# Kernel optimization log

Measured on AMD Instinct MI355X. Metric: run time of the kernel, lower is better.

## Reference

```python
import jax, jax.numpy as jnp
import numpy as np

N_FEATURES = 128
N_QUBITS = 10
Q_DEPTH = 4
N_OUTPUTS = 1
BATCH = 32768


def _apply_1q(psi, U, w, n):
    """Apply a single-qubit gate on wire w. psi: [B, 2^n]; U: [2,2] or [B,2,2]."""
    B = psi.shape[0]
    left, right = 2 ** w, 2 ** (n - 1 - w)
    psi = psi.reshape(B, left, 2, right)
    if U.ndim == 2:
        psi = jnp.einsum('ij,bljr->blir', U, psi)
    else:
        psi = jnp.einsum('bij,bljr->blir', U, psi)
    return psi.reshape(B, -1)


def _apply_cnot(psi, c, t, n):
    """CNOT(control=c, target=t) on psi [B, 2^n] (wire 0 = most significant bit)."""
    B = psi.shape[0]
    psi = psi.reshape((B,) + (2,) * n)
    ax_c, ax_t = c + 1, t + 1
    psi0 = jnp.take(psi, 0, axis=ax_c)
    psi1 = jnp.take(psi, 1, axis=ax_c)
    ax_t2 = ax_t - 1 if ax_t > ax_c else ax_t  # target axis shifts after removing control axis
    psi1 = jnp.flip(psi1, axis=ax_t2)          # flip target bit where control == 1
    psi = jnp.stack([psi0, psi1], axis=ax_c)
    return psi.reshape(B, -1)


def _rx_batched(theta):
    """RX(theta) per sample. theta: [B] -> U: [B,2,2] complex64."""
    c = jnp.cos(0.5 * theta).astype(jnp.complex64)
    s = jnp.sin(0.5 * theta).astype(jnp.complex64)
    row0 = jnp.stack([c, -1j * s], axis=-1)
    row1 = jnp.stack([-1j * s, c], axis=-1)
    return jnp.stack([row0, row1], axis=-2)


def _rot(phi, theta, omega):
    """Pennylane Rot = RZ(omega) @ RY(theta) @ RZ(phi), scalar angles -> [2,2] complex64."""
    c = jnp.cos(0.5 * theta)
    s = jnp.sin(0.5 * theta)
    u00 = jnp.exp(-0.5j * (phi + omega)) * c
    u01 = -jnp.exp(0.5j * (phi - omega)) * s
    u10 = jnp.exp(-0.5j * (phi - omega)) * s
    u11 = jnp.exp(0.5j * (phi + omega)) * c
    return jnp.stack([jnp.stack([u00, u01]), jnp.stack([u10, u11])]).astype(jnp.complex64)


def _quantum_forward(angles, q_weights):
    """Batched statevector sim: AngleEmbedding(RX) + StronglyEntanglingLayers, PauliZ expvals."""
    B, n = angles.shape
    depth = q_weights.shape[0]
    D = 2 ** n
    psi = jnp.zeros((B, D), jnp.complex64).at[:, 0].set(1.0)
    # AngleEmbedding: RX(angles[:, w]) on each wire (per-sample angles)
    for w in range(n):
        psi = _apply_1q(psi, _rx_batched(angles[:, w]), w, n)
    # StronglyEntanglingLayers: Rot on each wire, then CNOT ring with range r
    for l in range(depth):
        for w in range(n):
            U = _rot(q_weights[l, w, 0], q_weights[l, w, 1], q_weights[l, w, 2])
            psi = _apply_1q(psi, U, w, n)
        r = (l % (n - 1)) + 1
        for w in range(n):
            psi = _apply_cnot(psi, w, (w + r) % n, n)
    probs = psi.real ** 2 + psi.imag ** 2  # [B, D]
    # <Z_i> = sum_k probs[:,k] * (+1 if bit_i(k)==0 else -1); wire 0 = MSB
    bits = (jnp.arange(D)[None, :] >> (n - 1 - jnp.arange(n))[:, None]) & 1  # [n, D]
    signs = (1.0 - 2.0 * bits).astype(jnp.float32)
    return probs @ signs.T  # [B, n]


def setup_inputs() -> dict:
    key = jax.random.key(0)
    ks = jax.random.split(key, 5)
    x = jax.random.normal(ks[0], (BATCH, N_FEATURES), jnp.float32)
    W_pre = jax.random.normal(ks[1], (N_QUBITS, N_FEATURES), jnp.float32) / np.sqrt(N_FEATURES).astype(np.float32)
    b_pre = jnp.zeros((N_QUBITS,), jnp.float32)
    q_weights = 0.01 * jax.random.normal(ks[2], (Q_DEPTH, N_QUBITS, 3), jnp.float32)
    W_post = jax.random.normal(ks[3], (N_OUTPUTS, N_QUBITS), jnp.float32) / np.sqrt(N_QUBITS).astype(np.float32)
    b_post = jnp.zeros((N_OUTPUTS,), jnp.float32)
    return {"x": x, "W_pre": W_pre, "b_pre": b_pre, "q_weights": q_weights, "W_post": W_post, "b_post": b_post}


def reference(x, W_pre, b_pre, q_weights, W_post, b_post):
    angles = jnp.tanh(x @ W_pre.T + b_pre)        # pre_net + tanh -> [B, n_qubits]
    q_out = _quantum_forward(angles, q_weights)   # PauliZ expectations [B, n_qubits]
    return jax.nn.sigmoid(q_out @ W_post.T + b_post)
```

## Files before the change

kernel.cpp:

```cpp
#include <hip/hip_runtime.h>
#include <math.h>

#define BATCH 32768

typedef unsigned int u32;

#if defined(__has_builtin)
#if __has_builtin(__builtin_amdgcn_permlane32_swap) && __has_builtin(__builtin_amdgcn_permlane16_swap)
#define USE_PERMLANE 1
#else
#define USE_PERMLANE 0
#endif
#if __has_builtin(__builtin_amdgcn_fdot2)
#define HAS_FDOT2 1
#else
#define HAS_FDOT2 0
#endif
#else
#define USE_PERMLANE 0
#define HAS_FDOT2 0
#endif

struct GateC { unsigned prt, sel; };
struct CircuitT { GateC g[4][10]; unsigned srow[10]; };

constexpr CircuitT make_circuit() {
  CircuitT C{};
  unsigned row[10], col[10];
  for (int b = 0; b < 10; ++b) { row[b] = 1u << b; col[b] = 1u << b; }
  for (int l = 0; l < 4; ++l) {
    for (int w = 0; w < 10; ++w) {
      C.g[l][w].prt = col[9 - w];
      C.g[l][w].sel = row[9 - w];
    }
    const int r = (l % 9) + 1;
    for (int w = 0; w < 10; ++w) {
      const int c = w, t = (w + r) % 10;
      const int bc = 9 - c, bt = 9 - t;
      row[bt] ^= row[bc];
      col[bc] ^= col[bt];
    }
  }
  for (int i = 0; i < 10; ++i) C.srow[i] = row[9 - i];
  return C;
}
constexpr CircuitT CIRC = make_circuit();

constexpr int ORD[4][10] = {
  {0,1,2,3,4,5,6,7,8,9},
  {0,6,1,7,2,8,3,4,9,5},
  {0,2,1,3,7,4,8,5,9,6},
  {0,3,1,2,4,5,6,7,8,9},
};

template<int M>
__device__ __forceinline__ u32 lshuf(u32 v, int lane, int bpa) {
  static_assert(M != 0, "mask must be nonzero");
  if constexpr ((M & 32) != 0) {
    return (u32)__builtin_amdgcn_ds_bpermute(bpa, (int)v);
  } else {
    return (u32)__builtin_amdgcn_ds_swizzle((int)v, 0x1F | (M << 10));
  }
}

template<int CTRL>
__device__ __forceinline__ float dppf(float v) {
  const int i = __float_as_int(v);
  return __int_as_float(__builtin_amdgcn_update_dpp(i, i, CTRL, 0xF, 0xF, false));
}
__device__ __forceinline__ float shflx(float v, int m) { return __shfl_xor(v, m, 64); }

__device__ __forceinline__ float wave_sum(float v, int lane) {
  v += dppf<0xB1>(v);
  v += dppf<0x4E>(v);
  v += dppf<0x141>(v);
  v += dppf<0x140>(v);
#if USE_PERMLANE
  { auto r = __builtin_amdgcn_permlane16_swap(__float_as_uint(v), __float_as_uint(v), false, false);
    v = __uint_as_float(r[0]) + __uint_as_float(r[1]); }
  { auto r = __builtin_amdgcn_permlane32_swap(__float_as_uint(v), __float_as_uint(v), false, false);
    v = __uint_as_float(r[0]) + __uint_as_float(r[1]); }
#else
  v += shflx(v, 16);
  v += shflx(v, 32);
#endif
  return v;
}

__device__ __forceinline__ float half_sum(float v) {
  v += dppf<0xB1>(v);
  v += dppf<0x4E>(v);
  v += dppf<0x141>(v);
  v += dppf<0x140>(v);
#if USE_PERMLANE
  { auto r = __builtin_amdgcn_permlane16_swap(__float_as_uint(v), __float_as_uint(v), false, false);
    v = __uint_as_float(r[0]) + __uint_as_float(r[1]); }
#else
  v += shflx(v, 16);
#endif
  return v;
}

__device__ __forceinline__ float xswapf(float v, int lane) {
#if USE_PERMLANE
  auto r = __builtin_amdgcn_permlane32_swap(__float_as_uint(v), __float_as_uint(v), false, false);
  return (lane & 32) ? __uint_as_float(r[0]) : __uint_as_float(r[1]);
#else
  return shflx(v, 32);
#endif
}

__device__ __forceinline__ u32 pk_mul_h(u32 a, u32 b) {
  u32 d; asm("v_pk_mul_f16 %0, %1, %2" : "=v"(d) : "v"(a), "v"(b)); return d;
}
__device__ __forceinline__ u32 pk_fma_h(u32 a, u32 b, u32 c) {
  u32 d; asm("v_pk_fma_f16 %0, %1, %2, %3" : "=v"(d) : "v"(a), "v"(b), "v"(c)); return d;
}
__device__ __forceinline__ u32 pk_fma_hsw(u32 a, u32 b, u32 c) {
  u32 d;
  asm("v_pk_fma_f16 %0, %1, %2, %3 op_sel:[1,0,0] op_sel_hi:[0,1,1]"
      : "=v"(d) : "v"(a), "v"(b), "v"(c));
  return d;
}
__device__ __forceinline__ u32 pk2(float lo, float hi) {
  auto h = __builtin_amdgcn_cvt_pkrtz(lo, hi);
  return __builtin_bit_cast(u32, h);
}
__device__ __forceinline__ u32 updh(u32 a, u32 q, const uint4 s) {
  u32 t = pk_mul_h(a, s.x);
  t = pk_fma_hsw(a, s.y, t);
  t = pk_fma_h(q, s.z, t);
  t = pk_fma_hsw(q, s.w, t);
  return t;
}

template<int L, int W>
__device__ __forceinline__ void gate2(u32 a0[16], u32 a1[16],
                                      const u32* __restrict__ Ush, int lane) {
  constexpr unsigned PRT = CIRC.g[L][W].prt;
  constexpr unsigned SEL = CIRC.g[L][W].sel;
  constexpr int PLm = (int)(PRT >> 4), PRm = (int)(PRT & 15u);
  constexpr int SLm = (int)(SEL >> 4), SRm = (int)(SEL & 15u);

  int hl = 0;
  if constexpr (SLm != 0) hl = __popc(lane & SLm) & 1;

  const u32* gb = Ush + (L * 10 + W - 10) * 8;
  const uint4 cA = *(const uint4*)(gb + (hl << 2));
  uint4 cB;
  if constexpr (SRm != 0) cB = *(const uint4*)(gb + ((hl ^ 1) << 2));
  else                    cB = cA;

  int bpa = 0;
  if constexpr ((PLm & 32) != 0) bpa = (lane ^ PLm) << 2;

  if constexpr (PLm == 0) {
    constexpr int LB = PRm & (-PRm);
#pragma unroll
    for (int t0 = 0; t0 < 16; ++t0) {
      if (t0 & LB) continue;
      const int t1 = t0 ^ PRm;
      const uint4 s0 = (__builtin_popcount((unsigned)(t0 & SRm)) & 1) ? cB : cA;
      const uint4 s1 = (__builtin_popcount((unsigned)(t1 & SRm)) & 1) ? cB : cA;
      const u32 x0 = a0[t0], x1 = a0[t1];
      a0[t0] = updh(x0, x1, s0);
      a0[t1] = updh(x1, x0, s1);
      const u32 y0 = a1[t0], y1 = a1[t1];
      a1[t0] = updh(y0, y1, s0);
      a1[t1] = updh(y1, y0, s1);
    }
  } else {
#pragma unroll
    for (int t = 0; t < 16; ++t) {
      const uint4 s = (__builtin_popcount((unsigned)(t & SRm)) & 1) ? cB : cA;
      const u32 q0 = lshuf<PLm>(a0[t ^ PRm], lane, bpa);
      const u32 q1 = lshuf<PLm>(a1[t ^ PRm], lane, bpa);
      a0[t] = updh(a0[t], q0, s);
      a1[t] = updh(a1[t], q1, s);
    }
  }
}

template<int L, int K>
__device__ __forceinline__ void layer2_from(u32 a0[16], u32 a1[16],
                                            const u32* __restrict__ Ush, int lane) {
  if constexpr (K < 10) {
    gate2<L, ORD[L][K]>(a0, a1, Ush, lane);
    layer2_from<L, K + 1>(a0, a1, Ush, lane);
  }
}

__device__ __forceinline__ void build_state(u32 a[16], const float cw[10], const float sw[10],
                                            const u32* __restrict__ Ush, int lane) {
  float u0r[10], u0i[10], u1r[10], u1i[10];
#pragma unroll
  for (int w = 0; w < 10; ++w) {
    const u32* q = &Ush[240 + w * 8];
    const float A = __uint_as_float(q[0]), Br = __uint_as_float(q[1]);
    const float Bi = __uint_as_float(q[2]), Cr = __uint_as_float(q[3]);
    const float Ci = __uint_as_float(q[4]), Dr = __uint_as_float(q[5]);
    const float Di = __uint_as_float(q[6]);
    const float ch = cw[w], sh = sw[w];
    u0r[w] = fmaf(A, ch, Bi * sh);
    u0i[w] = -Br * sh;
    u1r[w] = fmaf(Cr, ch, Di * sh);
    u1i[w] = fmaf(Ci, ch, -Dr * sh);
  }

  float Lr, Li;
  {
    const int b0 = (lane >> 5) & 1;
    Lr = b0 ? u1r[0] : u0r[0];
    Li = b0 ? u1i[0] : u0i[0];
  }
#pragma unroll
  for (int w = 1; w < 6; ++w) {
    const int bb = (lane >> (5 - w)) & 1;
    const float arv = bb ? u1r[w] : u0r[w];
    const float aiv = bb ? u1i[w] : u0i[w];
    const float nr = fmaf(Lr, arv, -Li * aiv);
    const float ni = fmaf(Lr, aiv, Li * arv);
    Lr = nr; Li = ni;
  }

  float t4r[4], t4i[4], lsr[4], lsi[4];
#pragma unroll
  for (int aa = 0; aa < 2; ++aa) {
#pragma unroll
    for (int c2 = 0; c2 < 2; ++c2) {
      const int k = (aa << 1) | c2;
      const float ar6 = aa ? u1r[6] : u0r[6], ai6 = aa ? u1i[6] : u0i[6];
      const float ar7 = c2 ? u1r[7] : u0r[7], ai7 = c2 ? u1i[7] : u0i[7];
      t4r[k] = fmaf(ar6, ar7, -ai6 * ai7);
      t4i[k] = fmaf(ar6, ai7, ai6 * ar7);
      const float ar8 = aa ? u1r[8] : u0r[8], ai8 = aa ? u1i[8] : u0i[8];
      const float ar9 = c2 ? u1r[9] : u0r[9], ai9 = c2 ? u1i[9] : u0i[9];
      const float s4r = fmaf(ar8, ar9, -ai8 * ai9);
      const float s4i = fmaf(ar8, ai9, ai8 * ar9);
      lsr[k] = fmaf(s4r, Lr, -s4i * Li);
      lsi[k] = fmaf(s4r, Li, s4i * Lr);
    }
  }

#pragma unroll
  for (int t = 0; t < 16; ++t) {
    const int hi4 = t >> 2, lo4 = t & 3;
    const float re = fmaf(t4r[hi4], lsr[lo4], -t4i[hi4] * lsi[lo4]);
    const float im = fmaf(t4r[hi4], lsi[lo4],  t4i[hi4] * lsr[lo4]);
    a[t] = pk2(re, im);
  }
}

__global__ __launch_bounds__(256, 4) void qnn_kernel(
    const float* __restrict__ x, const float* __restrict__ Wpre,
    const float* __restrict__ bpre, const float* __restrict__ qw,
    const float* __restrict__ Wpost, const float* __restrict__ bpost,
    float* __restrict__ out)
{
  __shared__ __align__(16) u32 Ush[320];
  __shared__ float gtab[16 * 64];

  const int tid = threadIdx.x;
  if (tid < 40) {
    const float phi = qw[tid * 3 + 0];
    const float th  = qw[tid * 3 + 1];
    const float om  = qw[tid * 3 + 2];
    const float c = cosf(0.5f * th), s_ = sinf(0.5f * th);
    const float A  = c;
    const float Br = -cosf(phi) * s_, Bi = -sinf(phi) * s_;
    const float Cr =  cosf(om)  * s_, Ci =  sinf(om)  * s_;
    const float Dr =  cosf(phi + om) * c, Di = sinf(phi + om) * c;
    if (tid < 10) {
      u32* q = &Ush[240 + tid * 8];
      q[0] = __float_as_uint(A);  q[1] = __float_as_uint(Br);
      q[2] = __float_as_uint(Bi); q[3] = __float_as_uint(Cr);
      q[4] = __float_as_uint(Ci); q[5] = __float_as_uint(Dr);
      q[6] = __float_as_uint(Di); q[7] = 0u;
    } else {
      u32* p = &Ush[(tid - 10) * 8];
      p[0] = pk2(A, A);   p[1] = pk2(0.f, 0.f);
      p[2] = pk2(Br, Br); p[3] = pk2(-Bi, Bi);
      p[4] = pk2(Dr, Dr); p[5] = pk2(-Di, Di);
      p[6] = pk2(Cr, Cr); p[7] = pk2(-Ci, Ci);
    }
  }
#pragma unroll
  for (int k = 0; k < 4; ++k) {
    const int idx = tid * 4 + k;
    const int t = idx >> 6;
    const int l6 = idx & 63;
    float g = 0.f;
#pragma unroll
    for (int i = 0; i < 10; ++i) {
      const int sl = (int)(CIRC.srow[i] >> 4);
      const int sr = (int)(CIRC.srow[i] & 15u);
      const int par = (__popc(l6 & sl) + __popc(t & sr)) & 1;
      const float wv = Wpost[i];
      g += par ? -wv : wv;
    }
    gtab[t * 64 + l6] = g;
  }
  __syncthreads();

  const int lane = tid & 63;
  const int wid = tid >> 6;
  const int half = lane >> 5;
  const int hl5 = lane & 31;
  const int b0 = blockIdx.x * 8 + wid * 2;

  const float* xr = x + (size_t)(b0 + half) * 128;
  float xv[4];
#pragma unroll
  for (int k = 0; k < 4; ++k) xv[k] = xr[hl5 + 32 * k];

  float cw0[10], sw0[10], cw1[10], sw1[10];
#pragma unroll
  for (int w = 0; w < 10; ++w) {
    float p = 0.f;
#pragma unroll
    for (int k = 0; k < 4; ++k)
      p = fmaf(xv[k], Wpre[w * 128 + hl5 + 32 * k], p);
    p = half_sum(p);
    const float e = __expf(2.f * (p + bpre[w]));
    const float ang = 1.f - 2.f * __builtin_amdgcn_rcpf(e + 1.f);
    const float h = 0.5f * ang;
    const float c_own = __cosf(h);
    const float s_own = __sinf(h);
    const float c_oth = xswapf(c_own, lane);
    const float s_oth = xswapf(s_own, lane);
    cw0[w] = half ? c_oth : c_own;
    sw0[w] = half ? s_oth : s_own;
    cw1[w] = half ? c_own : c_oth;
    sw1[w] = half ? s_own : s_oth;
  }

  u32 a0[16], a1[16];
  build_state(a0, cw0, sw0, Ush, lane);
  build_state(a1, cw1, sw1, Ush, lane);

  layer2_from<1, 0>(a0, a1, Ush, lane);
  layer2_from<2, 0>(a0, a1, Ush, lane);
  layer2_from<3, 0>(a0, a1, Ush, lane);

  float acc0 = 0.f, acc1 = 0.f;
#pragma unroll
  for (int t = 0; t < 16; ++t) {
    const float g = gtab[t * 64 + lane];
#if HAS_FDOT2
    typedef _Float16 h2 __attribute__((ext_vector_type(2)));
    const h2 ah0 = __builtin_bit_cast(h2, a0[t]);
    const h2 ah1 = __builtin_bit_cast(h2, a1[t]);
    acc0 = fmaf(__builtin_amdgcn_fdot2(ah0, ah0, 0.f, false), g, acc0);
    acc1 = fmaf(__builtin_amdgcn_fdot2(ah1, ah1, 0.f, false), g, acc1);
#else
    union H2U { u32 u; _Float16 h[2]; } z0, z1;
    z0.u = a0[t]; z1.u = a1[t];
    const float r0 = (float)z0.h[0], i0 = (float)z0.h[1];
    const float r1 = (float)z1.h[0], i1 = (float)z1.h[1];
    acc0 = fmaf(fmaf(r0, r0, i0 * i0), g, acc0);
    acc1 = fmaf(fmaf(r1, r1, i1 * i1), g, acc1);
#endif
  }
  acc0 = wave_sum(acc0, lane);
  acc1 = wave_sum(acc1, lane);

  if (lane == 0) {
    const float bp = bpost[0];
    out[b0]     = __builtin_amdgcn_rcpf(1.f + __expf(-(acc0 + bp)));
    out[b0 + 1] = __builtin_amdgcn_rcpf(1.f + __expf(-(acc1 + bp)));
  }
}

extern "C" void kernel_launch(void* const* d_in, const int* in_sizes, int n_in,
                              void* d_out, int out_size, void* d_ws, size_t ws_size,
                              hipStream_t stream) {
  const float* x     = (const float*)d_in[0];
  const float* Wpre  = (const float*)d_in[1];
  const float* bpre  = (const float*)d_in[2];
  const float* qw    = (const float*)d_in[3];
  const float* Wpost = (const float*)d_in[4];
  const float* bpost = (const float*)d_in[5];
  float* out = (float*)d_out;

  (void)in_sizes; (void)n_in; (void)out_size; (void)d_ws; (void)ws_size;

  qnn_kernel<<<BATCH / 8, 256, 0, stream>>>(x, Wpre, bpre, qw, Wpost, bpost, out);
}
```

Before: 155.3 us.

## Precompute gate constants and parity table in a setup kernel via workspace

Moves the per-block trig evaluation of gate coefficients and the Wpost parity-table computation into a single tiny setup kernel that writes them to the workspace. Each main block then only copies them into shared memory with vector loads. The main kernel's launch bounds are also raised from 4 to 8 blocks per CU. The setup runs every call, so it is not caching across calls, but it adds a second launch and a dependency, and the higher occupancy target may force register spills.

```diff
diff --git a/kernel.cpp b/kernel.cpp
--- a/kernel.cpp
+++ b/kernel.cpp
@@ -52,6 +52,8 @@
   {0,2,1,3,7,4,8,5,9,6},
   {0,3,1,2,4,5,6,7,8,9},
 };
+
+#define WS_WORDS 1344
 
 template<int M>
 __device__ __forceinline__ u32 lshuf(u32 v, int lane, int bpa) {
@@ -132,6 +134,58 @@
   t = pk_fma_h(q, s.z, t);
   t = pk_fma_hsw(q, s.w, t);
   return t;
+}
+
+__device__ __forceinline__ void compute_gate_words(int g, const float* __restrict__ qw,
+                                                   u32* __restrict__ dst ) {
+  const float phi = qw[g * 3 + 0];
+  const float th  = qw[g * 3 + 1];
+  const float om  = qw[g * 3 + 2];
+  const float c = cosf(0.5f * th), s_ = sinf(0.5f * th);
+  const float A  = c;
+  const float Br = -cosf(phi) * s_, Bi = -sinf(phi) * s_;
+  const float Cr =  cosf(om)  * s_, Ci =  sinf(om)  * s_;
+  const float Dr =  cosf(phi + om) * c, Di = sinf(phi + om) * c;
+  if (g < 10) {
+    u32* q = dst + 240 + g * 8;
+    q[0] = __float_as_uint(A);  q[1] = __float_as_uint(Br);
+    q[2] = __float_as_uint(Bi); q[3] = __float_as_uint(Cr);
+    q[4] = __float_as_uint(Ci); q[5] = __float_as_uint(Dr);
+    q[6] = __float_as_uint(Di); q[7] = 0u;
+  } else {
+    u32* p = dst + (g - 10) * 8;
+    p[0] = pk2(A, A);   p[1] = pk2(0.f, 0.f);
+    p[2] = pk2(Br, Br); p[3] = pk2(-Bi, Bi);
+    p[4] = pk2(Dr, Dr); p[5] = pk2(-Di, Di);
+    p[6] = pk2(Cr, Cr); p[7] = pk2(-Ci, Ci);
+  }
+}
+
+__device__ __forceinline__ float compute_gtab_entry(int idx, const float* __restrict__ Wpost) {
+  const int t = idx >> 6;
+  const int l6 = idx & 63;
+  float g = 0.f;
+#pragma unroll
+  for (int i = 0; i < 10; ++i) {
+    const int sl = (int)(CIRC.srow[i] >> 4);
+    const int sr = (int)(CIRC.srow[i] & 15u);
+    const int par = (__popc(l6 & sl) + __popc(t & sr)) & 1;
+    const float wv = Wpost[i];
+    g += par ? -wv : wv;
+  }
+  return g;
+}
+
+__global__ void qnn_setup(const float* __restrict__ qw, const float* __restrict__ Wpost,
+                          u32* __restrict__ ws) {
+  const int tid = threadIdx.x;
+  if (tid < 40) compute_gate_words(tid, qw, ws);
+  float* gt = (float*)(ws + 320);
+#pragma unroll
+  for (int k = 0; k < 16; ++k) {
+    const int idx = k * 64 + tid;
+    gt[idx] = compute_gtab_entry(idx, Wpost);
+  }
 }
 
 template<int L, int W>
@@ -251,54 +305,27 @@
   }
 }
 
-__global__ __launch_bounds__(256, 4) void qnn_kernel(
+template<bool FROMWS>
+__global__ __launch_bounds__(256, 8) void qnn_kernel(
     const float* __restrict__ x, const float* __restrict__ Wpre,
     const float* __restrict__ bpre, const float* __restrict__ qw,
     const float* __restrict__ Wpost, const float* __restrict__ bpost,
-    float* __restrict__ out)
+    const u32* __restrict__ ws, float* __restrict__ out)
 {
   __shared__ __align__(16) u32 Ush[320];
-  __shared__ float gtab[16 * 64];
+  __shared__ __align__(16) float gtab[16 * 64];
 
   const int tid = threadIdx.x;
-  if (tid < 40) {
-    const float phi = qw[tid * 3 + 0];
-    const float th  = qw[tid * 3 + 1];
-    const float om  = qw[tid * 3 + 2];
-    const float c = cosf(0.5f * th), s_ = sinf(0.5f * th);
-    const float A  = c;
-    const float Br = -cosf(phi) * s_, Bi = -sinf(phi) * s_;
-    const float Cr =  cosf(om)  * s_, Ci =  sinf(om)  * s_;
-    const float Dr =  cosf(phi + om) * c, Di = sinf(phi + om) * c;
-    if (tid < 10) {
-      u32* q = &Ush[240 + tid * 8];
-      q[0] = __float_as_uint(A);  q[1] = __float_as_uint(Br);
-      q[2] = __float_as_uint(Bi); q[3] = __float_as_uint(Cr);
-      q[4] = __float_as_uint(Ci); q[5] = __float_as_uint(Dr);
-      q[6] = __float_as_uint(Di); q[7] = 0u;
-    } else {
-      u32* p = &Ush[(tid - 10) * 8];
-      p[0] = pk2(A, A);   p[1] = pk2(0.f, 0.f);
-      p[2] = pk2(Br, Br); p[3] = pk2(-Bi, Bi);
-      p[4] = pk2(Dr, Dr); p[5] = pk2(-Di, Di);
-      p[6] = pk2(Cr, Cr); p[7] = pk2(-Ci, Ci);
-    }
-  }
-#pragma unroll
-  for (int k = 0; k < 4; ++k) {
-    const int idx = tid * 4 + k;
-    const int t = idx >> 6;
-    const int l6 = idx & 63;
-    float g = 0.f;
-#pragma unroll
-    for (int i = 0; i < 10; ++i) {
-      const int sl = (int)(CIRC.srow[i] >> 4);
-      const int sr = (int)(CIRC.srow[i] & 15u);
-      const int par = (__popc(l6 & sl) + __popc(t & sr)) & 1;
-      const float wv = Wpost[i];
-      g += par ? -wv : wv;
-    }
-    gtab[t * 64 + l6] = g;
+  if constexpr (FROMWS) {
+    if (tid < 80) ((uint4*)Ush)[tid] = ((const uint4*)ws)[tid];
+    ((float4*)gtab)[tid] = ((const float4*)(ws + 320))[tid];
+  } else {
+    if (tid < 40) compute_gate_words(tid, qw, Ush);
+#pragma unroll
+    for (int k = 0; k < 4; ++k) {
+      const int idx = tid * 4 + k;
+      gtab[idx] = compute_gtab_entry(idx, Wpost);
+    }
   }
   __syncthreads();
 
@@ -381,8 +408,14 @@
   const float* Wpost = (const float*)d_in[4];
   const float* bpost = (const float*)d_in[5];
   float* out = (float*)d_out;
-
-  (void)in_sizes; (void)n_in; (void)out_size; (void)d_ws; (void)ws_size;
-
-  qnn_kernel<<<BATCH / 8, 256, 0, stream>>>(x, Wpre, bpre, qw, Wpost, bpost, out);
-}
+  u32* ws = (u32*)d_ws;
+
+  (void)in_sizes; (void)n_in; (void)out_size;
+
+  if (ws_size >= WS_WORDS * sizeof(u32)) {
+    qnn_setup<<<1, 64, 0, stream>>>(qw, Wpost, ws);
+    qnn_kernel<true><<<BATCH / 8, 256, 0, stream>>>(x, Wpre, bpre, qw, Wpost, bpost, ws, out);
+  } else {
+    qnn_kernel<false><<<BATCH / 8, 256, 0, stream>>>(x, Wpre, bpre, qw, Wpost, bpost, ws, out);
+  }
+}
```

Measured after the change: 176.3 us. 13.5% more time.
